# Performance work log

Hardware: AMD Instinct MI355X
Metric: run time of the kernel (lower is better)

The kernel has to match this reference:

```python
import jax, jax.numpy as jnp
import numpy as np

NEG = jnp.float32(-1e30)  # log-space -inf surrogate (safe for grads)


def _ctc_neg_log_likelihood(logprobs, labels, input_lens, label_lens):
    """CTC forward (alpha) recursion, blank=0.
    logprobs: (T, N, V) log-softmax outputs; labels: (N, L) int; lens: (N,).
    Returns per-sample negative log-likelihood (N,).
    """
    T, N, V = logprobs.shape
    L = labels.shape[1]
    S = 2 * L + 1
    # Extended label sequence: blank, l1, blank, l2, ..., blank
    z = jnp.zeros((N, S), dtype=labels.dtype).at[:, 1::2].set(labels)
    # Per-step emission log-probs for extended labels: (T, N, S)
    lp = logprobs[:, jnp.arange(N)[:, None], z]
    # Skip connection s-2 -> s allowed iff z[s] != blank and z[s] != z[s-2]
    z_m2 = jnp.pad(z, ((0, 0), (2, 0)))[:, :S]
    skip = (z != 0) & (z != z_m2)
    skip = skip.at[:, :2].set(False)

    alpha0 = jnp.full((N, S), NEG, dtype=logprobs.dtype)
    alpha0 = alpha0.at[:, 0].set(lp[0, :, 0]).at[:, 1].set(lp[0, :, 1])

    def step(alpha, xs):
        lp_t, t = xs
        a1 = jnp.pad(alpha, ((0, 0), (1, 0)), constant_values=NEG)[:, :S]
        a2 = jnp.pad(alpha, ((0, 0), (2, 0)), constant_values=NEG)[:, :S]
        a2 = jnp.where(skip, a2, NEG)
        new = jnp.logaddexp(jnp.logaddexp(alpha, a1), a2) + lp_t
        # Freeze alpha once past each sample's input length
        new = jnp.where((t < input_lens)[:, None], new, alpha)
        return new, None

    ts = jnp.arange(1, T)
    alpha, _ = jax.lax.scan(step, alpha0, (lp[1:], ts))

    idx_blank = (2 * label_lens).astype(jnp.int32)  # final blank position
    end1 = jnp.take_along_axis(alpha, idx_blank[:, None], axis=1)[:, 0]
    end2 = jnp.take_along_axis(alpha, (idx_blank - 1)[:, None], axis=1)[:, 0]
    return -jnp.logaddexp(end1, end2)


def setup_inputs() -> dict:
    key = jax.random.key(0)
    k1, k2, k3, k4, k5 = jax.random.split(key, 5)
    N, T, D, V, L = 16, 512, 512, 4096, 128
    encoder_out = jax.random.normal(k1, (N, T, D), dtype=jnp.float32)
    W = jax.random.normal(k2, (D, V), dtype=jnp.float32) / jnp.sqrt(jnp.float32(D))
    b = jnp.zeros((V,), dtype=jnp.float32)
    encoder_out_lens = jax.random.randint(k3, (N,), 300, T + 1, dtype=jnp.int32)
    padded_labels = jax.random.randint(k4, (N, L), 1, V, dtype=jnp.int32)
    label_lengths = jax.random.randint(k5, (N,), 64, L + 1, dtype=jnp.int32)
    return {
        "encoder_out": encoder_out,
        "W": W,
        "b": b,
        "encoder_out_lens": encoder_out_lens,
        "padded_labels": padded_labels,
        "label_lengths": label_lengths,
    }


def reference(encoder_out, W, b, encoder_out_lens, padded_labels, label_lengths):
    # Dropout is identity in eval mode. proj -> (N, T, V)
    logits = jnp.einsum("ntd,dv->ntv", encoder_out, W) + b
    # transpose(0,1).log_softmax(2) -> (T, N, V)
    logprobs = jax.nn.log_softmax(logits.transpose(1, 0, 2), axis=2)
    nll = _ctc_neg_log_likelihood(logprobs, padded_labels, encoder_out_lens, label_lengths)
    # reduction='sum', then divided by batch size
    return jnp.sum(nll) / padded_labels.shape[0]
```

## Files before the change

kernel.cpp:

```cpp
#include <hip/hip_runtime.h>

#define NEGF (-1e30f)
#define LOG2E 1.4426950408889634f
#define LN2d  0.6931471805599453

typedef __attribute__((ext_vector_type(8))) short bf16x8;
typedef __attribute__((ext_vector_type(4))) float f32x4;

__device__ __forceinline__ unsigned short f2bf(float x) {
  unsigned u = __float_as_uint(x);
  unsigned r = (u + 0x7FFFu + ((u >> 16) & 1u)) >> 16;
  return (unsigned short)r;
}


__device__ __forceinline__ void d_cvtx(int bid, int tid,
                                       const float* __restrict__ X,
                                       unsigned short* __restrict__ Xbf) {
  const int i = bid * 256 + tid;
  float4 v = ((const float4*)X)[i];
  ushort4 h;
  h.x = f2bf(v.x); h.y = f2bf(v.y); h.z = f2bf(v.z); h.w = f2bf(v.w);
  ((ushort4*)Xbf)[i] = h;
}

__device__ __forceinline__ void d_gather(int bid, int tid,
                                         const float* __restrict__ W,
                                         const float* __restrict__ b,
                                         const int* __restrict__ labels,
                                         float* __restrict__ Wgt,
                                         float* __restrict__ gb) {
  const int n  = bid >> 7;
  const int kc = bid & 127;
  const int k0 = kc << 2;
  for (int idx = tid; idx < 4 * 129; idx += 256) {
    const int kk = idx / 129;
    const int j  = idx - kk * 129;
    const int c  = (j == 0) ? 0 : labels[n * 128 + (j - 1)];
    const int k  = k0 + kk;
    Wgt[((size_t)(n * 512 + k)) * 132 + j] = W[(size_t)k * 4096 + c];
    if (kc == 0 && kk == 0) gb[n * 129 + j] = b[c];
  }
}

__device__ __forceinline__ void d_wtrans(int bid, int tid, char* smem,
                                         const float* __restrict__ W,
                                         unsigned short* __restrict__ Wt) {
  float (*tile)[65] = (float (*)[65])smem;
  const int kb = bid & 7;
  const int vb = bid >> 3;
  const int k0 = kb << 6, v0 = vb << 6;
#pragma unroll
  for (int it = 0; it < 16; ++it) {
    const int idx = it * 256 + tid;
    const int r = idx >> 6, c = idx & 63;
    tile[r][c] = W[(size_t)(k0 + r) * 4096 + v0 + c];
  }
  __syncthreads();
#pragma unroll
  for (int it = 0; it < 16; ++it) {
    const int idx = it * 256 + tid;
    const int vr = idx >> 6, kc = idx & 63;
    Wt[(size_t)(v0 + vr) * 512 + k0 + kc] = f2bf(tile[kc][vr]);
  }
}

__device__ __forceinline__ void stage_tile(const unsigned short* __restrict__ src,
                                           int r0, char* ldsbase, int wave,
                                           int tid, int kbyte) {
#pragma unroll
  for (int j = 0; j < 2; ++j) {
    const int chunk = (tid & 3) ^ ((tid >> 3) & 3);
    const char* gp = (const char*)src +
        (size_t)(r0 + j * 64 + (tid >> 2)) * 1024 + kbyte + chunk * 16;
    char* lp = ldsbase + j * 4096 + wave * 1024;
    __builtin_amdgcn_global_load_lds(
        (const __attribute__((address_space(1))) unsigned int*)gp,
        (__attribute__((address_space(3))) unsigned int*)lp, 16, 0, 0);
  }
}

__device__ __forceinline__ void d_gemm(int gid, int tid, char* smem,
                                       const unsigned short* __restrict__ Xbf,
                                       const unsigned short* __restrict__ Wt,
                                       const float* __restrict__ bvec,
                                       const int* __restrict__ lens,
                                       float* __restrict__ pg) {
  const int bm = gid >> 5;
  const int bn = gid & 31;
  const int n  = bm >> 2;
  const int t0 = (bm & 3) << 7;
  if (t0 >= lens[n]) return;
  const int m0 = bm << 7;
  const int v0 = bn << 7;

  const int wave = tid >> 6;
  const int lane = tid & 63;
  const int lrow = lane & 15;
  const int lk   = (lane >> 4) * 16;
  const int lks  = lk ^ (((lrow >> 1) & 3) << 4);
  const int wr   = wave >> 1;
  const int wn   = wave & 1;

  f32x4 acc[4][4];
#pragma unroll
  for (int mi = 0; mi < 4; ++mi)
#pragma unroll
    for (int ni = 0; ni < 4; ++ni) acc[mi][ni] = (f32x4){0.f, 0.f, 0.f, 0.f};

  {
    char* buf = smem;
    stage_tile(Xbf, m0, buf + 0,    wave, tid, 0);
    stage_tile(Wt,  v0, buf + 8192, wave, tid, 0);
  }
  __syncthreads();

  int cur = 0;
  for (int kk = 0; kk < 16; ++kk) {
    if (kk < 15) {
      char* nbuf = smem + (cur ^ 1) * 16384;
      const int kb = (kk + 1) << 6;
      stage_tile(Xbf, m0, nbuf + 0,    wave, tid, kb);
      stage_tile(Wt,  v0, nbuf + 8192, wave, tid, kb);
    }
    const char* buf = smem + cur * 16384;
    bf16x8 ah[4], bh[4];
#pragma unroll
    for (int mi = 0; mi < 4; ++mi) {
      const int off = (wr * 64 + mi * 16 + lrow) * 64 + lks;
      ah[mi] = *(const bf16x8*)(buf + off);
    }
#pragma unroll
    for (int ni = 0; ni < 4; ++ni) {
      const int off = (wn * 64 + ni * 16 + lrow) * 64 + lks;
      bh[ni] = *(const bf16x8*)(buf + 8192 + off);
    }
#pragma unroll
    for (int mi = 0; mi < 4; ++mi)
#pragma unroll
      for (int ni = 0; ni < 4; ++ni)
        acc[mi][ni] = __builtin_amdgcn_mfma_f32_16x16x32_bf16(ah[mi], bh[ni], acc[mi][ni], 0, 0, 0);
    __syncthreads();
    cur ^= 1;
  }

  const float lg2e = LOG2E;
  float bias[4];
#pragma unroll
  for (int ni = 0; ni < 4; ++ni) bias[ni] = bvec[v0 + wn * 64 + ni * 16 + lrow];
  float* part = (float*)(smem + 32768);
#pragma unroll
  for (int mi = 0; mi < 4; ++mi)
#pragma unroll
    for (int reg = 0; reg < 4; ++reg) {
      float s = 0.f;
#pragma unroll
      for (int ni = 0; ni < 4; ++ni)
        s += exp2f((acc[mi][ni][reg] + bias[ni]) * lg2e);
#pragma unroll
      for (int msk = 1; msk < 16; msk <<= 1) s += __shfl_xor(s, msk);
      if (lrow == 0)
        part[(wr * 64 + mi * 16 + (lane >> 4) * 4 + reg) * 2 + wn] = s;
    }
  __syncthreads();
  if (tid < 128)
    pg[(size_t)(m0 + tid) * 32 + bn] = part[tid * 2 + 0] + part[tid * 2 + 1];
}

__device__ __forceinline__ float lae32(float x, float y, float z) {
  float m = fmaxf(fmaxf(x, y), z);
  float e = exp2f(x - m) + exp2f(y - m) + exp2f(z - m);
  return m + __log2f(e);
}

__device__ __forceinline__ float lae3n(float x, float y, float z) {
  float m = fmaxf(fmaxf(x, y), z);
  float e = __expf(x - m) + __expf(y - m) + __expf(z - m);
  return m + __logf(e);
}

__device__ __forceinline__ void stage32(const float* __restrict__ gsrc,
                                        char* ldsbase, int tid, int wave) {
#pragma unroll
  for (int k = 0; k < 4; ++k) {
    const char* gp = (const char*)gsrc + k * 4096 + (size_t)tid * 16;
    char* lp = ldsbase + k * 4096 + wave * 1024;
    __builtin_amdgcn_global_load_lds(
        (const __attribute__((address_space(1))) unsigned int*)gp,
        (__attribute__((address_space(3))) unsigned int*)lp, 16, 0, 0);
  }
  if (tid < 32) {
    const char* gp = (const char*)gsrc + 16384 + (size_t)tid * 16;
    char* lp = ldsbase + 16384;
    __builtin_amdgcn_global_load_lds(
        (const __attribute__((address_space(1))) unsigned int*)gp,
        (__attribute__((address_space(3))) unsigned int*)lp, 16, 0, 0);
  }
}

__device__ void d_scan(int sbid, int tid, char* smem,
                       const float* __restrict__ g,
                       const int* __restrict__ labels,
                       const int* __restrict__ in_lens,
                       const int* __restrict__ lab_lens,
                       float* __restrict__ af,
                       float* __restrict__ ab) {
  const int n    = sbid >> 1;
  const int dir  = sbid & 1;
  const int wave = tid >> 6;
  const int l    = tid & 63;
  const int len  = in_lens[n];
  const int tm   = len >> 1;
  const float* gn = g + (size_t)n * 512 * 132;
  const int s0 = 5 * l;

  int jm0, jm1, jm2, jm3, jm4;
  {
    int jmv[5];
#pragma unroll
    for (int i = 0; i < 5; ++i) {
      const int s = s0 + i;
      jmv[i] = (s < 257 && (s & 1)) ? ((s + 1) >> 1) : 0;
    }
    jm0 = jmv[0]; jm1 = jmv[1]; jm2 = jmv[2]; jm3 = jmv[3]; jm4 = jmv[4];
  }

  if (dir == 0) {
    bool sk0, sk1, sk2, sk3, sk4;
    {
      bool skv[5];
#pragma unroll
      for (int i = 0; i < 5; ++i) {
        const int s = s0 + i;
        skv[i] = false;
        if (s < 257 && (s & 1) && s >= 3) {
          const int li = (s - 1) >> 1;
          const int cl = labels[n * 128 + li];
          skv[i] = (cl != 0) && (cl != labels[n * 128 + li - 1]);
        }
      }
      sk0 = skv[0]; sk1 = skv[1]; sk2 = skv[2]; sk3 = skv[3]; sk4 = skv[4];
    }
    stage32(gn, smem, tid, wave);
    __syncthreads();

    float a0 = NEGF, a1 = NEGF, a2 = NEGF, a3 = NEGF, a4 = NEGF;
    if (tid < 64 && l == 0) {
      const float* B0 = (const float*)smem;
      a0 = B0[0]; a1 = B0[1];
    }
    float a3p = NEGF, a4p = NEGF;

    int t = 1, c = 0;
    while (true) {
      const bool more = ((c + 1) << 5) <= tm;
      if (more)
        stage32(gn + (size_t)((c + 1) << 5) * 132,
                smem + ((c + 1) & 1) * 16896, tid, wave);
      if (tid < 64) {
        const float* B = (const float*)(smem + (c & 1) * 16896);
        const int ce = (c << 5) + 31;
        const int tend = (tm < ce) ? tm : ce;
        int ro = (t - (c << 5)) * 132;
        float p0 = B[ro + jm0], p1 = B[ro + jm1], p2 = B[ro + jm2],
              p3 = B[ro + jm3], p4 = B[ro + jm4];
        for (; t <= tend; ++t) {
          const int ro2 = (t < tend) ? ro + 132 : ro;
          const float q0 = B[ro2 + jm0];
          const float q1 = B[ro2 + jm1];
          const float q2 = B[ro2 + jm2];
          const float q3 = B[ro2 + jm3];
          const float q4 = B[ro2 + jm4];
          float x3 = a3p, x4 = a4p;
          if (l == 0) { x3 = NEGF; x4 = NEGF; }
          const float n3 = lae32(a3, a2, sk3 ? a1 : NEGF) + p3;
          const float n4 = lae32(a4, a3, sk4 ? a2 : NEGF) + p4;
          a3p = __shfl_up(n3, 1);
          a4p = __shfl_up(n4, 1);
          const float n0 = lae32(a0, x4, sk0 ? x3 : NEGF) + p0;
          const float n1 = lae32(a1, a0, sk1 ? x4 : NEGF) + p1;
          const float n2 = lae32(a2, a1, sk2 ? a0 : NEGF) + p2;
          a0 = n0; a1 = n1; a2 = n2; a3 = n3; a4 = n4;
          p0 = q0; p1 = q1; p2 = q2; p3 = q3; p4 = q4;
          ro = ro2;
        }
      }
      if (!more) break;
      __syncthreads();
      ++c;
    }
    if (tid < 64) {
      float* o = af + n * 320 + s0;
      o[0] = a0; o[1] = a1; o[2] = a2; o[3] = a3; o[4] = a4;
    }
  } else {
    bool skd0, skd1, skd2, skd3, skd4;
    {
      bool skv[5];
#pragma unroll
      for (int i = 0; i < 5; ++i) {
        const int s2 = s0 + i + 2;
        skv[i] = false;
        if (s2 < 257 && (s2 & 1) && s2 >= 3) {
          const int li = (s2 - 1) >> 1;
          const int cl = labels[n * 128 + li];
          skv[i] = (cl != 0) && (cl != labels[n * 128 + li - 1]);
        }
      }
      skd0 = skv[0]; skd1 = skv[1]; skd2 = skv[2]; skd3 = skv[3]; skd4 = skv[4];
    }
    int c = (len - 1) >> 5;
    stage32(gn + (size_t)(c << 5) * 132, smem + (c & 1) * 16896, tid, wave);
    __syncthreads();

    float b0, b1, b2, b3, b4;
    {
      const int ll = lab_lens[n];
      const int i1 = 2 * ll, i2 = 2 * ll - 1;
      b0 = (s0 + 0 == i1 || s0 + 0 == i2) ? 0.f : NEGF;
      b1 = (s0 + 1 == i1 || s0 + 1 == i2) ? 0.f : NEGF;
      b2 = (s0 + 2 == i1 || s0 + 2 == i2) ? 0.f : NEGF;
      b3 = (s0 + 3 == i1 || s0 + 3 == i2) ? 0.f : NEGF;
      b4 = (s0 + 4 == i1 || s0 + 4 == i2) ? 0.f : NEGF;
    }

    int t = len - 2;
    while (true) {
      const bool more = (c << 5) > tm + 1;
      if (more)
        stage32(gn + (size_t)((c - 1) << 5) * 132,
                smem + ((c - 1) & 1) * 16896, tid, wave);
      if (tid < 64) {
        const float* B = (const float*)(smem + (c & 1) * 16896);
        const int cl0 = (c << 5) - 1;
        const int tlo = (tm > cl0) ? tm : cl0;
        int ro = (t + 1 - (c << 5)) * 132;
        float p0 = B[ro + jm0], p1 = B[ro + jm1], p2 = B[ro + jm2],
              p3 = B[ro + jm3], p4 = B[ro + jm4];
        for (; t >= tlo; --t) {
          const int ro2 = (t - 1 >= tlo) ? ro - 132 : ro;
          const float q0 = B[ro2 + jm0];
          const float q1 = B[ro2 + jm1];
          const float q2 = B[ro2 + jm2];
          const float q3 = B[ro2 + jm3];
          const float q4 = B[ro2 + jm4];
          const float c0 = b0 + p0;
          const float c1 = b1 + p1;
          float c5 = __shfl_down(c0, 1);
          float c6 = __shfl_down(c1, 1);
          const float c2 = b2 + p2;
          const float c3 = b3 + p3;
          const float c4 = b4 + p4;
          const float m0n = lae32(c0, c1, skd0 ? c2 : NEGF);
          const float m1n = lae32(c1, c2, skd1 ? c3 : NEGF);
          const float m2n = lae32(c2, c3, skd2 ? c4 : NEGF);
          if (l == 63) { c5 = NEGF; c6 = NEGF; }
          const float m3n = lae32(c3, c4, skd3 ? c5 : NEGF);
          const float m4n = lae32(c4, c5, skd4 ? c6 : NEGF);
          b0 = m0n; b1 = m1n; b2 = m2n; b3 = m3n; b4 = m4n;
          p0 = q0; p1 = q1; p2 = q2; p3 = q3; p4 = q4;
          ro = ro2;
        }
      }
      if (!more) break;
      __syncthreads();
      --c;
    }
    if (tid < 64) {
      float* o = ab + n * 320 + s0;
      o[0] = b0; o[1] = b1; o[2] = b2; o[3] = b3; o[4] = b4;
    }
  }
}


__global__ __launch_bounds__(256) void k_prep1(const float* __restrict__ X,
                                               unsigned short* __restrict__ Xbf,
                                               const float* __restrict__ W,
                                               const float* __restrict__ b,
                                               const int* __restrict__ labels,
                                               float* __restrict__ Wgt,
                                               float* __restrict__ gb,
                                               unsigned short* __restrict__ Wt) {
  __shared__ __align__(16) char smem[16640];
  const int bid = blockIdx.x;
  if (bid < 4096)      d_cvtx(bid, threadIdx.x, X, Xbf);
  else if (bid < 6144) d_gather(bid - 4096, threadIdx.x, W, b, labels, Wgt, gb);
  else                 d_wtrans(bid - 6144, threadIdx.x, smem, W, Wt);
}

__global__ __launch_bounds__(256) void k_glp8(const float* __restrict__ X,
                                              const float* __restrict__ Wgt,
                                              const float* __restrict__ gb,
                                              const int* __restrict__ lens,
                                              float* __restrict__ g) {
  __shared__ float xs[8][512];
  const int bid = blockIdx.x;
  const int n  = bid >> 6;
  const int r0 = (bid & 63) << 3;
  if (r0 >= lens[n]) return;
  const int m0 = n * 512 + r0;
  {
    const float4* Xv = (const float4*)(X + (size_t)m0 * 512);
    float4* xsv = (float4*)(&xs[0][0]);
    for (int i = threadIdx.x; i < 8 * 128; i += 256) xsv[i] = Xv[i];
  }
  __syncthreads();
  const int j = threadIdx.x;
  if (j >= 129) return;
  const float* wp = Wgt + (size_t)(n * 512) * 132 + j;
  float acc[8];
#pragma unroll
  for (int r = 0; r < 8; ++r) acc[r] = 0.f;
  float w0 = wp[0], w1 = wp[132], w2 = wp[264], w3 = wp[396];
  for (int k4 = 0; k4 < 128; ++k4) {
    const int kn = (k4 + 1) & 127;
    float p0 = wp[(size_t)(kn * 4 + 0) * 132];
    float p1 = wp[(size_t)(kn * 4 + 1) * 132];
    float p2 = wp[(size_t)(kn * 4 + 2) * 132];
    float p3 = wp[(size_t)(kn * 4 + 3) * 132];
#pragma unroll
    for (int r = 0; r < 8; ++r) {
      float4 x4 = *(const float4*)(&xs[r][k4 << 2]);
      acc[r] = fmaf(x4.x, w0, acc[r]);
      acc[r] = fmaf(x4.y, w1, acc[r]);
      acc[r] = fmaf(x4.z, w2, acc[r]);
      acc[r] = fmaf(x4.w, w3, acc[r]);
    }
    w0 = p0; w1 = p1; w2 = p2; w3 = p3;
  }
  const float bb = gb[n * 129 + j];
#pragma unroll
  for (int r = 0; r < 8; ++r)
    g[(size_t)(m0 + r) * 132 + j] = (acc[r] + bb) * LOG2E;
}

__global__ __launch_bounds__(256, 4) void k_main(const float* __restrict__ g,
                                                 const int* __restrict__ labels,
                                                 const int* __restrict__ in_lens,
                                                 const int* __restrict__ lab_lens,
                                                 float* __restrict__ af,
                                                 float* __restrict__ ab,
                                                 const unsigned short* __restrict__ Xbf,
                                                 const unsigned short* __restrict__ Wt,
                                                 const float* __restrict__ bvec,
                                                 float* __restrict__ pg) {
  __shared__ __align__(16) char smem[33792];
  const int bid = blockIdx.x;
  if (bid < 32) {
    d_scan(bid, threadIdx.x, smem, g, labels, in_lens, lab_lens, af, ab);
  } else {
    d_gemm(bid - 32, threadIdx.x, smem, Xbf, Wt, bvec, in_lens, pg);
  }
}

__global__ __launch_bounds__(256) void k_tail(const float* __restrict__ pg,
                                              const int* __restrict__ lens,
                                              const float* __restrict__ af,
                                              const float* __restrict__ ab,
                                              float* __restrict__ nll) {
  const int n = blockIdx.x, tid = threadIdx.x;
  const int len = lens[n];
  __shared__ double red[256];
  double s = 0.0;
  for (int t = tid; t < len; t += 256) {
    const float4* p = (const float4*)(pg + ((size_t)(n * 512 + t)) * 32);
    float e = 0.f;
#pragma unroll
    for (int i = 0; i < 8; ++i) { float4 v = p[i]; e += v.x + v.y + v.z + v.w; }
    s += (double)__logf(e);
  }
  red[tid] = s;
  __syncthreads();
  for (int off = 128; off > 0; off >>= 1) {
    if (tid < off) red[tid] += red[tid + off];
    __syncthreads();
  }
  if (tid < 64) {
    const int l = tid;
    const int s0 = 5 * l;
    float v0 = NEGF, v1 = NEGF, v2 = NEGF, v3 = NEGF, v4 = NEGF;
    const float* f = af + n * 320 + s0;
    const float* bb = ab + n * 320 + s0;
    if (s0 + 0 < 257) v0 = f[0] + bb[0];
    if (s0 + 1 < 257) v1 = f[1] + bb[1];
    if (s0 + 2 < 257) v2 = f[2] + bb[2];
    if (s0 + 3 < 257) v3 = f[3] + bb[3];
    if (s0 + 4 < 257) v4 = f[4] + bb[4];
    float M = fmaxf(fmaxf(v0, v1), fmaxf(fmaxf(v2, v3), v4));
#pragma unroll
    for (int off = 1; off < 64; off <<= 1) M = fmaxf(M, __shfl_xor(M, off));
    float e = exp2f(v0 - M) + exp2f(v1 - M) + exp2f(v2 - M)
            + exp2f(v3 - M) + exp2f(v4 - M);
#pragma unroll
    for (int off = 1; off < 64; off <<= 1) e += __shfl_xor(e, off);
    if (l == 0)
      nll[n] = (float)(red[0] - (double)(M + __log2f(e)) * LN2d);
  }
}

__global__ void k_finish(const float* __restrict__ nll, float* __restrict__ out) {
  const int l = threadIdx.x;
  float v = (l < 16) ? nll[l] : 0.f;
#pragma unroll
  for (int off = 8; off > 0; off >>= 1) v += __shfl_down(v, off);
  if (l == 0) out[0] = v * 0.0625f;
}

__global__ void k_gather_w(const float* __restrict__ W,
                           const float* __restrict__ b,
                           const int* __restrict__ labels,
                           float* __restrict__ Wgt,
                           float* __restrict__ gb) {
  d_gather(blockIdx.x, threadIdx.x, W, b, labels, Wgt, gb);
}

__global__ __launch_bounds__(256) void k_glp(const float* __restrict__ X,
                                             const float* __restrict__ Wgt,
                                             const float* __restrict__ gb,
                                             const float* __restrict__ lse,
                                             const int* __restrict__ lens,
                                             float* __restrict__ g) {
  const int blk = blockIdx.x;
  const int n   = blk >> 4;
  const int t0  = (blk & 15) << 5;
  if (t0 >= lens[n]) return;
  const int m0 = n * 512 + t0;
  __shared__ float xs[32][512];
  {
    const float4* Xv = (const float4*)(X + (size_t)m0 * 512);
    float4* xsv = (float4*)(&xs[0][0]);
    for (int i = threadIdx.x; i < 32 * 128; i += 256) xsv[i] = Xv[i];
  }
  __syncthreads();
  const int j = threadIdx.x;
  if (j >= 129) return;
  const float* wp = Wgt + (size_t)(n * 512) * 132 + j;
  float acc[32];
#pragma unroll
  for (int r = 0; r < 32; ++r) acc[r] = 0.f;
  float w0 = wp[0], w1 = wp[132], w2 = wp[264], w3 = wp[396];
  for (int k4 = 0; k4 < 128; ++k4) {
    const int kn = (k4 + 1) & 127;
    float p0 = wp[(size_t)(kn * 4 + 0) * 132];
    float p1 = wp[(size_t)(kn * 4 + 1) * 132];
    float p2 = wp[(size_t)(kn * 4 + 2) * 132];
    float p3 = wp[(size_t)(kn * 4 + 3) * 132];
#pragma unroll
    for (int r = 0; r < 32; ++r) {
      float4 x4 = *(const float4*)(&xs[r][k4 << 2]);
      acc[r] = fmaf(x4.x, w0, acc[r]);
      acc[r] = fmaf(x4.y, w1, acc[r]);
      acc[r] = fmaf(x4.z, w2, acc[r]);
      acc[r] = fmaf(x4.w, w3, acc[r]);
    }
    w0 = p0; w1 = p1; w2 = p2; w3 = p3;
  }
  const float bb = gb[n * 129 + j];
#pragma unroll
  for (int r = 0; r < 32; ++r)
    g[(size_t)(m0 + r) * 132 + j] = acc[r] + bb - lse[m0 + r];
}

__global__ void k_ctc_g(const float* __restrict__ g,
                        const int* __restrict__ labels,
                        const int* __restrict__ in_lens,
                        const int* __restrict__ lab_lens,
                        float* __restrict__ nll) {
  const int n = blockIdx.x;
  const int l = threadIdx.x;
  const float* gn = g + (size_t)n * 512 * 132;
  const int len = in_lens[n];
  const int s0 = 5 * l;
  int jm[5]; bool sk[5];
#pragma unroll
  for (int i = 0; i < 5; ++i) {
    const int s = s0 + i;
    const bool valid = (s < 257);
    jm[i] = (valid && (s & 1)) ? ((s + 1) >> 1) : 0;
    sk[i] = false;
    if (valid && (s & 1) && s >= 3) {
      const int li = (s - 1) >> 1;
      const int cl = labels[n * 128 + li];
      sk[i] = (cl != 0) && (cl != labels[n * 128 + li - 1]);
    }
  }
  float a[5];
  a[0] = (l == 0) ? gn[0] : NEGF;
  a[1] = (l == 0) ? gn[1] : NEGF;
  a[2] = NEGF; a[3] = NEGF; a[4] = NEGF;
  float lp[5];
#pragma unroll
  for (int i = 0; i < 5; ++i) lp[i] = gn[132 + jm[i]];
  for (int t = 1; t < len; ++t) {
    const int tp = (t + 1 < len) ? (t + 1) : t;
    float np[5];
#pragma unroll
    for (int i = 0; i < 5; ++i) np[i] = gn[(size_t)tp * 132 + jm[i]];
    float a3p = __shfl_up(a[3], 1);
    float a4p = __shfl_up(a[4], 1);
    if (l == 0) { a3p = NEGF; a4p = NEGF; }
    const float b0 = lae3n(a[0], a4p,  sk[0] ? a3p  : NEGF) + lp[0];
    const float b1 = lae3n(a[1], a[0], sk[1] ? a4p  : NEGF) + lp[1];
    const float b2 = lae3n(a[2], a[1], sk[2] ? a[0] : NEGF) + lp[2];
    const float b3 = lae3n(a[3], a[2], sk[3] ? a[1] : NEGF) + lp[3];
    const float b4 = lae3n(a[4], a[3], sk[4] ? a[2] : NEGF) + lp[4];
    a[0] = b0; a[1] = b1; a[2] = b2; a[3] = b3; a[4] = b4;
#pragma unroll
    for (int i = 0; i < 5; ++i) lp[i] = np[i];
  }
  __shared__ float al[320];
#pragma unroll
  for (int i = 0; i < 5; ++i) al[s0 + i] = a[i];
  __syncthreads();
  if (l == 0) {
    const int ll  = lab_lens[n];
    const int idx = 2 * ll;
    const float e1 = al[idx], e2 = al[idx - 1];
    const float m = fmaxf(e1, e2);
    const float r = m + __logf(__expf(e1 - m) + __expf(e2 - m));
    nll[n] = -r;
  }
}

__global__ __launch_bounds__(512, 2) void k_lse(const float* __restrict__ X,
                                                const float* __restrict__ W,
                                                const float* __restrict__ b,
                                                const int* __restrict__ lens,
                                                float* __restrict__ lse,
                                                float* __restrict__ red_g) {
  const int blk = blockIdx.x;
  const int n   = blk >> 4;
  const int t0  = (blk & 15) << 5;
  if (t0 >= lens[n]) return;
  const int m0 = n * 512 + t0;
  __shared__ float xs[32][512];
  {
    const float4* Xv = (const float4*)(X + (size_t)m0 * 512);
    float4* xsv = (float4*)(&xs[0][0]);
    for (int i = threadIdx.x; i < 32 * 128; i += 512) xsv[i] = Xv[i];
  }
  float* redb = red_g + (size_t)blk * 256;
  for (int i = threadIdx.x; i < 256; i += 512) redb[i] = 0.f;
  __syncthreads();
  const int wave = threadIdx.x >> 6;
  const int lane = threadIdx.x & 63;
  for (int j = 0; j < 4; ++j) {
    const int v = (j << 10) + (threadIdx.x << 1);
    const float* Wv = W + v;
    float2 acc[32];
#pragma unroll
    for (int r = 0; r < 32; ++r) acc[r] = make_float2(0.f, 0.f);
    float2 w0 = *(const float2*)(Wv + 0 * 4096);
    float2 w1 = *(const float2*)(Wv + 1 * 4096);
    float2 w2 = *(const float2*)(Wv + 2 * 4096);
    float2 w3 = *(const float2*)(Wv + 3 * 4096);
    for (int k4 = 0; k4 < 128; ++k4) {
      const int kn = (k4 + 1) & 127;
      float2 p0 = *(const float2*)(Wv + (kn * 4 + 0) * 4096);
      float2 p1 = *(const float2*)(Wv + (kn * 4 + 1) * 4096);
      float2 p2 = *(const float2*)(Wv + (kn * 4 + 2) * 4096);
      float2 p3 = *(const float2*)(Wv + (kn * 4 + 3) * 4096);
#pragma unroll
      for (int r = 0; r < 32; ++r) {
        float4 x4 = *(const float4*)(&xs[r][k4 << 2]);
        acc[r].x = fmaf(x4.x, w0.x, acc[r].x);
        acc[r].y = fmaf(x4.x, w0.y, acc[r].y);
        acc[r].x = fmaf(x4.y, w1.x, acc[r].x);
        acc[r].y = fmaf(x4.y, w1.y, acc[r].y);
        acc[r].x = fmaf(x4.z, w2.x, acc[r].x);
        acc[r].y = fmaf(x4.z, w2.y, acc[r].y);
        acc[r].x = fmaf(x4.w, w3.x, acc[r].x);
        acc[r].y = fmaf(x4.w, w3.y, acc[r].y);
      }
      w0 = p0; w1 = p1; w2 = p2; w3 = p3;
    }
    const float2 bb = *(const float2*)(b + v);
#pragma unroll
    for (int r = 0; r < 32; ++r) {
      float e = __expf(acc[r].x + bb.x) + __expf(acc[r].y + bb.y);
#pragma unroll
      for (int off = 32; off > 0; off >>= 1) e += __shfl_xor(e, off);
      if (lane == 0) redb[wave * 32 + r] += e;
    }
  }
  __syncthreads();
  if (threadIdx.x < 32) {
    float s = 0.f;
#pragma unroll
    for (int w = 0; w < 8; ++w) s += redb[w * 32 + threadIdx.x];
    lse[m0 + threadIdx.x] = __logf(s);
  }
}

extern "C" void kernel_launch(void* const* d_in, const int* in_sizes, int n_in,
                              void* d_out, int out_size, void* d_ws, size_t ws_size,
                              hipStream_t stream) {
  const float* X        = (const float*)d_in[0];
  const float* W        = (const float*)d_in[1];
  const float* b        = (const float*)d_in[2];
  const int*   in_lens  = (const int*)d_in[3];
  const int*   labels   = (const int*)d_in[4];
  const int*   lab_lens = (const int*)d_in[5];
  float* out = (float*)d_out;
  char* wsb = (char*)d_ws;

  const size_t NEED = 34906240;
  if (ws_size >= NEED) {
    float* pg  = (float*)(wsb + 32768);
    float* Wgt = (float*)(wsb + 1081344);
    float* gb  = (float*)(wsb + 5406720);
    float* g   = (float*)(wsb + 5414976);
    float* nll = (float*)(wsb + 9740352);
    unsigned short* Xbf = (unsigned short*)(wsb + 9740416);
    unsigned short* Wt  = (unsigned short*)(wsb + 18129024);
    float* af = (float*)(wsb + 26517632);
    float* ab = (float*)(wsb + 26517632 + 20480);

    k_prep1<<<dim3(6656), dim3(256), 0, stream>>>(X, Xbf, W, b, labels, Wgt, gb, Wt);
    k_glp8<<<dim3(1024), dim3(256), 0, stream>>>(X, Wgt, gb, in_lens, g);
    k_main<<<dim3(2080), dim3(256), 0, stream>>>(g, labels, in_lens, lab_lens,
                                                 af, ab, Xbf, Wt, b, pg);
    k_tail<<<dim3(16), dim3(256), 0, stream>>>(pg, in_lens, af, ab, nll);
    k_finish<<<dim3(1), dim3(64), 0, stream>>>(nll, out);
  } else {
    float* ws    = (float*)d_ws;
    float* lse   = ws;
    float* red_g = ws + 8192;
    float* Wgt   = ws + 8192 + 65536;
    float* gb    = Wgt + 1081344;
    float* g     = gb + 2064;
    float* nll   = g + 1081344;
    k_lse<<<dim3(256), dim3(512), 0, stream>>>(X, W, b, in_lens, lse, red_g);
    k_gather_w<<<dim3(2048), dim3(256), 0, stream>>>(W, b, labels, Wgt, gb);
    k_glp<<<dim3(256), dim3(256), 0, stream>>>(X, Wgt, gb, lse, in_lens, g);
    k_ctc_g<<<dim3(16), dim3(64), 0, stream>>>(g, labels, in_lens, lab_lens, nll);
    k_finish<<<dim3(1), dim3(64), 0, stream>>>(nll, out);
  }
}
```

Before: 168.9 us.

## Fuse label-logprob GEMM into main kernel with per-chunk counters feeding scan

Moves the gathered-label projection (k_glp8) into k_main as extra blocks. Each block bumps a per-chunk atomic counter when done, and the CTC scan blocks spin on those counters before staging each 32-step chunk. This lets the scan start as soon as its first chunks are ready instead of waiting for a separate kernel launch. It also merges k_tail and k_finish into one single-block kernel, removing a launch. The cost is spin-wait polling, and a deadlock risk if scan blocks are resident while the producer blocks cannot be scheduled; the low block indices of the scan and producers make that unlikely.

```diff
diff --git a/kernel.cpp b/kernel.cpp
--- a/kernel.cpp
+++ b/kernel.cpp
@@ -65,6 +65,61 @@
   }
 }
 
+__device__ void d_glp8(int idx, int tid, char* smem,
+                       const float* __restrict__ X,
+                       const float* __restrict__ Wgt,
+                       const float* __restrict__ gb,
+                       const int* __restrict__ lens,
+                       float* __restrict__ g,
+                       int* __restrict__ cnt) {
+  const int n  = idx >> 6;
+  const int r0 = (idx & 63) << 3;
+  const int fc = n * 16 + (r0 >> 5);
+  if (r0 >= lens[n]) {
+    if (tid == 0) atomicAdd(&cnt[fc], 1);
+    return;
+  }
+  const int m0 = n * 512 + r0;
+  float (*xs)[512] = (float (*)[512])smem;
+  {
+    const float4* Xv = (const float4*)(X + (size_t)m0 * 512);
+    float4* xsv = (float4*)(&xs[0][0]);
+    for (int i = tid; i < 8 * 128; i += 256) xsv[i] = Xv[i];
+  }
+  __syncthreads();
+  const int j = tid;
+  if (j < 129) {
+    const float* wp = Wgt + (size_t)(n * 512) * 132 + j;
+    float acc[8];
+#pragma unroll
+    for (int r = 0; r < 8; ++r) acc[r] = 0.f;
+    float w0 = wp[0], w1 = wp[132], w2 = wp[264], w3 = wp[396];
+    for (int k4 = 0; k4 < 128; ++k4) {
+      const int kn = (k4 + 1) & 127;
+      float p0 = wp[(size_t)(kn * 4 + 0) * 132];
+      float p1 = wp[(size_t)(kn * 4 + 1) * 132];
+      float p2 = wp[(size_t)(kn * 4 + 2) * 132];
+      float p3 = wp[(size_t)(kn * 4 + 3) * 132];
+#pragma unroll
+      for (int r = 0; r < 8; ++r) {
+        float4 x4 = *(const float4*)(&xs[r][k4 << 2]);
+        acc[r] = fmaf(x4.x, w0, acc[r]);
+        acc[r] = fmaf(x4.y, w1, acc[r]);
+        acc[r] = fmaf(x4.z, w2, acc[r]);
+        acc[r] = fmaf(x4.w, w3, acc[r]);
+      }
+      w0 = p0; w1 = p1; w2 = p2; w3 = p3;
+    }
+    const float bb = gb[n * 129 + j];
+#pragma unroll
+    for (int r = 0; r < 8; ++r)
+      g[(size_t)(m0 + r) * 132 + j] = (acc[r] + bb) * LOG2E;
+  }
+  __threadfence();
+  __syncthreads();
+  if (tid == 0) atomicAdd(&cnt[fc], 1);
+}
+
 __device__ __forceinline__ void stage_tile(const unsigned short* __restrict__ src,
                                            int r0, char* ldsbase, int wave,
                                            int tid, int kbyte) {
@@ -198,13 +253,21 @@
   }
 }
 
+__device__ __forceinline__ void waitchunk(int* cnt, int slot, int tid) {
+  if (tid == 0) {
+    while (atomicAdd(&cnt[slot], 0) < 4) { __builtin_amdgcn_s_sleep(8); }
+  }
+  __syncthreads();
+}
+
 __device__ void d_scan(int sbid, int tid, char* smem,
                        const float* __restrict__ g,
                        const int* __restrict__ labels,
                        const int* __restrict__ in_lens,
                        const int* __restrict__ lab_lens,
                        float* __restrict__ af,
-                       float* __restrict__ ab) {
+                       float* __restrict__ ab,
+                       int* __restrict__ cnt) {
   const int n    = sbid >> 1;
   const int dir  = sbid & 1;
   const int wave = tid >> 6;
@@ -241,6 +304,7 @@
       }
       sk0 = skv[0]; sk1 = skv[1]; sk2 = skv[2]; sk3 = skv[3]; sk4 = skv[4];
     }
+    waitchunk(cnt, n * 16, tid);
     stage32(gn, smem, tid, wave);
     __syncthreads();
 
@@ -254,9 +318,11 @@
     int t = 1, c = 0;
     while (true) {
       const bool more = ((c + 1) << 5) <= tm;
-      if (more)
+      if (more) {
+        waitchunk(cnt, n * 16 + c + 1, tid);
         stage32(gn + (size_t)((c + 1) << 5) * 132,
                 smem + ((c + 1) & 1) * 16896, tid, wave);
+      }
       if (tid < 64) {
         const float* B = (const float*)(smem + (c & 1) * 16896);
         const int ce = (c << 5) + 31;
@@ -310,6 +376,7 @@
       skd0 = skv[0]; skd1 = skv[1]; skd2 = skv[2]; skd3 = skv[3]; skd4 = skv[4];
     }
     int c = (len - 1) >> 5;
+    waitchunk(cnt, n * 16 + c, tid);
     stage32(gn + (size_t)(c << 5) * 132, smem + (c & 1) * 16896, tid, wave);
     __syncthreads();
 
@@ -327,9 +394,11 @@
     int t = len - 2;
     while (true) {
       const bool more = (c << 5) > tm + 1;
-      if (more)
+      if (more) {
+        waitchunk(cnt, n * 16 + c - 1, tid);
         stage32(gn + (size_t)((c - 1) << 5) * 132,
                 smem + ((c - 1) & 1) * 16896, tid, wave);
+      }
       if (tid < 64) {
         const float* B = (const float*)(smem + (c & 1) * 16896);
         const int cl0 = (c << 5) - 1;
@@ -381,61 +450,20 @@
                                                const int* __restrict__ labels,
                                                float* __restrict__ Wgt,
                                                float* __restrict__ gb,
-                                               unsigned short* __restrict__ Wt) {
+                                               unsigned short* __restrict__ Wt,
+                                               int* __restrict__ cnt) {
   __shared__ __align__(16) char smem[16640];
   const int bid = blockIdx.x;
   if (bid < 4096)      d_cvtx(bid, threadIdx.x, X, Xbf);
   else if (bid < 6144) d_gather(bid - 4096, threadIdx.x, W, b, labels, Wgt, gb);
-  else                 d_wtrans(bid - 6144, threadIdx.x, smem, W, Wt);
-}
-
-__global__ __launch_bounds__(256) void k_glp8(const float* __restrict__ X,
-                                              const float* __restrict__ Wgt,
-                                              const float* __restrict__ gb,
-                                              const int* __restrict__ lens,
-                                              float* __restrict__ g) {
-  __shared__ float xs[8][512];
-  const int bid = blockIdx.x;
-  const int n  = bid >> 6;
-  const int r0 = (bid & 63) << 3;
-  if (r0 >= lens[n]) return;
-  const int m0 = n * 512 + r0;
-  {
-    const float4* Xv = (const float4*)(X + (size_t)m0 * 512);
-    float4* xsv = (float4*)(&xs[0][0]);
-    for (int i = threadIdx.x; i < 8 * 128; i += 256) xsv[i] = Xv[i];
-  }
-  __syncthreads();
-  const int j = threadIdx.x;
-  if (j >= 129) return;
-  const float* wp = Wgt + (size_t)(n * 512) * 132 + j;
-  float acc[8];
-#pragma unroll
-  for (int r = 0; r < 8; ++r) acc[r] = 0.f;
-  float w0 = wp[0], w1 = wp[132], w2 = wp[264], w3 = wp[396];
-  for (int k4 = 0; k4 < 128; ++k4) {
-    const int kn = (k4 + 1) & 127;
-    float p0 = wp[(size_t)(kn * 4 + 0) * 132];
-    float p1 = wp[(size_t)(kn * 4 + 1) * 132];
-    float p2 = wp[(size_t)(kn * 4 + 2) * 132];
-    float p3 = wp[(size_t)(kn * 4 + 3) * 132];
-#pragma unroll
-    for (int r = 0; r < 8; ++r) {
-      float4 x4 = *(const float4*)(&xs[r][k4 << 2]);
-      acc[r] = fmaf(x4.x, w0, acc[r]);
-      acc[r] = fmaf(x4.y, w1, acc[r]);
-      acc[r] = fmaf(x4.z, w2, acc[r]);
-      acc[r] = fmaf(x4.w, w3, acc[r]);
-    }
-    w0 = p0; w1 = p1; w2 = p2; w3 = p3;
-  }
-  const float bb = gb[n * 129 + j];
-#pragma unroll
-  for (int r = 0; r < 8; ++r)
-    g[(size_t)(m0 + r) * 132 + j] = (acc[r] + bb) * LOG2E;
-}
-
-__global__ __launch_bounds__(256, 4) void k_main(const float* __restrict__ g,
+  else if (bid < 6656) d_wtrans(bid - 6144, threadIdx.x, smem, W, Wt);
+  else                 cnt[threadIdx.x] = 0;
+}
+
+__global__ __launch_bounds__(256, 4) void k_main(const float* __restrict__ X,
+                                                 const float* __restrict__ Wgt,
+                                                 const float* __restrict__ gb,
+                                                 float* __restrict__ g,
                                                  const int* __restrict__ labels,
                                                  const int* __restrict__ in_lens,
                                                  const int* __restrict__ lab_lens,
@@ -444,67 +472,72 @@
                                                  const unsigned short* __restrict__ Xbf,
                                                  const unsigned short* __restrict__ Wt,
                                                  const float* __restrict__ bvec,
-                                                 float* __restrict__ pg) {
+                                                 float* __restrict__ pg,
+                                                 int* __restrict__ cnt) {
   __shared__ __align__(16) char smem[33792];
   const int bid = blockIdx.x;
   if (bid < 32) {
-    d_scan(bid, threadIdx.x, smem, g, labels, in_lens, lab_lens, af, ab);
+    d_scan(bid, threadIdx.x, smem, g, labels, in_lens, lab_lens, af, ab, cnt);
+  } else if (bid < 1056) {
+    d_glp8(bid - 32, threadIdx.x, smem, X, Wgt, gb, in_lens, g, cnt);
   } else {
-    d_gemm(bid - 32, threadIdx.x, smem, Xbf, Wt, bvec, in_lens, pg);
-  }
-}
-
-__global__ __launch_bounds__(256) void k_tail(const float* __restrict__ pg,
-                                              const int* __restrict__ lens,
-                                              const float* __restrict__ af,
-                                              const float* __restrict__ ab,
-                                              float* __restrict__ nll) {
-  const int n = blockIdx.x, tid = threadIdx.x;
+    d_gemm(bid - 1056, threadIdx.x, smem, Xbf, Wt, bvec, in_lens, pg);
+  }
+}
+
+__global__ __launch_bounds__(256) void k_tail2(const float* __restrict__ pg,
+                                               const int* __restrict__ lens,
+                                               const float* __restrict__ af,
+                                               const float* __restrict__ ab,
+                                               float* __restrict__ out) {
+  const int tid = threadIdx.x;
+  const int n = tid >> 4, q = tid & 15;
   const int len = lens[n];
-  __shared__ double red[256];
+  __shared__ double redd[256];
+  __shared__ float  redf[256];
+  __shared__ double nsh[16];
   double s = 0.0;
-  for (int t = tid; t < len; t += 256) {
+  for (int t = q; t < len; t += 16) {
     const float4* p = (const float4*)(pg + ((size_t)(n * 512 + t)) * 32);
     float e = 0.f;
 #pragma unroll
     for (int i = 0; i < 8; ++i) { float4 v = p[i]; e += v.x + v.y + v.z + v.w; }
     s += (double)__logf(e);
   }
-  red[tid] = s;
-  __syncthreads();
-  for (int off = 128; off > 0; off >>= 1) {
-    if (tid < off) red[tid] += red[tid + off];
+  redd[tid] = s;
+  __syncthreads();
+  for (int off = 8; off > 0; off >>= 1) {
+    if (q < off) redd[tid] += redd[tid + off];
     __syncthreads();
   }
-  if (tid < 64) {
-    const int l = tid;
-    const int s0 = 5 * l;
-    float v0 = NEGF, v1 = NEGF, v2 = NEGF, v3 = NEGF, v4 = NEGF;
-    const float* f = af + n * 320 + s0;
-    const float* bb = ab + n * 320 + s0;
-    if (s0 + 0 < 257) v0 = f[0] + bb[0];
-    if (s0 + 1 < 257) v1 = f[1] + bb[1];
-    if (s0 + 2 < 257) v2 = f[2] + bb[2];
-    if (s0 + 3 < 257) v3 = f[3] + bb[3];
-    if (s0 + 4 < 257) v4 = f[4] + bb[4];
-    float M = fmaxf(fmaxf(v0, v1), fmaxf(fmaxf(v2, v3), v4));
-#pragma unroll
-    for (int off = 1; off < 64; off <<= 1) M = fmaxf(M, __shfl_xor(M, off));
-    float e = exp2f(v0 - M) + exp2f(v1 - M) + exp2f(v2 - M)
-            + exp2f(v3 - M) + exp2f(v4 - M);
-#pragma unroll
-    for (int off = 1; off < 64; off <<= 1) e += __shfl_xor(e, off);
-    if (l == 0)
-      nll[n] = (float)(red[0] - (double)(M + __log2f(e)) * LN2d);
-  }
-}
-
-__global__ void k_finish(const float* __restrict__ nll, float* __restrict__ out) {
-  const int l = threadIdx.x;
-  float v = (l < 16) ? nll[l] : 0.f;
-#pragma unroll
-  for (int off = 8; off > 0; off >>= 1) v += __shfl_down(v, off);
-  if (l == 0) out[0] = v * 0.0625f;
+  const float* f  = af + n * 320;
+  const float* bb = ab + n * 320;
+  float M = NEGF;
+  for (int st = q; st < 257; st += 16) M = fmaxf(M, f[st] + bb[st]);
+  redf[tid] = M;
+  __syncthreads();
+  for (int off = 8; off > 0; off >>= 1) {
+    if (q < off) redf[tid] = fmaxf(redf[tid], redf[tid + off]);
+    __syncthreads();
+  }
+  const float Mg = redf[n << 4];
+  __syncthreads();
+  float e = 0.f;
+  for (int st = q; st < 257; st += 16) e += exp2f(f[st] + bb[st] - Mg);
+  redf[tid] = e;
+  __syncthreads();
+  for (int off = 8; off > 0; off >>= 1) {
+    if (q < off) redf[tid] += redf[tid + off];
+    __syncthreads();
+  }
+  if (q == 0)
+    nsh[n] = redd[tid] - (double)(Mg + __log2f(redf[tid])) * LN2d;
+  __syncthreads();
+  if (tid == 0) {
+    double acc = 0.0;
+    for (int i = 0; i < 16; ++i) acc += nsh[i];
+    out[0] = (float)(acc * 0.0625);
+  }
 }
 
 __global__ void k_gather_w(const float* __restrict__ W,
@@ -693,6 +726,14 @@
   }
 }
 
+__global__ void k_finish(const float* __restrict__ nll, float* __restrict__ out) {
+  const int l = threadIdx.x;
+  float v = (l < 16) ? nll[l] : 0.f;
+#pragma unroll
+  for (int off = 8; off > 0; off >>= 1) v += __shfl_down(v, off);
+  if (l == 0) out[0] = v * 0.0625f;
+}
+
 extern "C" void kernel_launch(void* const* d_in, const int* in_sizes, int n_in,
                               void* d_out, int out_size, void* d_ws, size_t ws_size,
                               hipStream_t stream) {
@@ -707,22 +748,22 @@
 
   const size_t NEED = 34906240;
   if (ws_size >= NEED) {
+    int*   cnt = (int*)(wsb + 0);
     float* pg  = (float*)(wsb + 32768);
     float* Wgt = (float*)(wsb + 1081344);
     float* gb  = (float*)(wsb + 5406720);
     float* g   = (float*)(wsb + 5414976);
-    float* nll = (float*)(wsb + 9740352);
     unsigned short* Xbf = (unsigned short*)(wsb + 9740416);
     unsigned short* Wt  = (unsigned short*)(wsb + 18129024);
     float* af = (float*)(wsb + 26517632);
     float* ab = (float*)(wsb + 26517632 + 20480);
 
-    k_prep1<<<dim3(6656), dim3(256), 0, stream>>>(X, Xbf, W, b, labels, Wgt, gb, Wt);
-    k_glp8<<<dim3(1024), dim3(256), 0, stream>>>(X, Wgt, gb, in_lens, g);
-    k_main<<<dim3(2080), dim3(256), 0, stream>>>(g, labels, in_lens, lab_lens,
-                                                 af, ab, Xbf, Wt, b, pg);
-    k_tail<<<dim3(16), dim3(256), 0, stream>>>(pg, in_lens, af, ab, nll);
-    k_finish<<<dim3(1), dim3(64), 0, stream>>>(nll, out);
+    k_prep1<<<dim3(6657), dim3(256), 0, stream>>>(X, Xbf, W, b, labels, Wgt,
+                                                  gb, Wt, cnt);
+    k_main<<<dim3(3104), dim3(256), 0, stream>>>(X, Wgt, gb, g, labels,
+                                                 in_lens, lab_lens, af, ab,
+                                                 Xbf, Wt, b, pg, cnt);
+    k_tail2<<<dim3(1), dim3(256), 0, stream>>>(pg, in_lens, af, ab, out);
   } else {
     float* ws    = (float*)d_ws;
     float* lse   = ws;
```

Measured after the change: 294.8 us. 74.5% more time.
